# Performance work log

Hardware: AMD Instinct MI355X
Metric: run time of the kernel (lower is better)

## Reference

```python
import jax, jax.numpy as jnp
import numpy as np
from jax import lax

B, N, NPOINT, NSAMPLE = 16, 8192, 1024, 32
RADIUS = 0.2
EPS = 1e-5


def setup_inputs() -> dict:
    key = jax.random.key(0)
    ks = jax.random.split(key, 6)
    return {
        "xyz": jax.random.uniform(ks[0], (B, N, 3), dtype=jnp.float32),
        "points": jax.random.normal(ks[1], (B, N, 64), dtype=jnp.float32),
        "w1": jax.random.normal(ks[2], (64, 67), dtype=jnp.float32) * 0.1,
        "b1": jnp.zeros((64,), jnp.float32),
        "g1": jnp.ones((64,), jnp.float32),
        "be1": jnp.zeros((64,), jnp.float32),
        "w2": jax.random.normal(ks[3], (64, 64), dtype=jnp.float32) * 0.1,
        "b2": jnp.zeros((64,), jnp.float32),
        "g2": jnp.ones((64,), jnp.float32),
        "be2": jnp.zeros((64,), jnp.float32),
        "w3": jax.random.normal(ks[4], (128, 64), dtype=jnp.float32) * 0.1,
        "b3": jnp.zeros((128,), jnp.float32),
        "g3": jnp.ones((128,), jnp.float32),
        "be3": jnp.zeros((128,), jnp.float32),
    }


def farthest_point_sample(xyz, npoint):
    # Sequential FPS; deterministic start at index 0 (torch uses a random start).
    b, n, _ = xyz.shape
    batch_ix = jnp.arange(b)

    def step(carry, _):
        distance, farthest = carry
        centroid = xyz[batch_ix, farthest]              # [B,3]
        dist = jnp.sum((xyz - centroid[:, None, :]) ** 2, -1)  # [B,N]
        distance = jnp.minimum(distance, dist)
        return (distance, jnp.argmax(distance, -1).astype(jnp.int32)), farthest

    init = (jnp.full((b, n), 1e10, jnp.float32), jnp.zeros((b,), jnp.int32))
    _, idxs = lax.scan(step, init, None, length=npoint)
    return idxs.T                                        # [B,npoint]


def gather_points(points, idx):
    # points [B,N,C], idx [B,...] -> [B,...,C]
    return jax.vmap(lambda p, i: p[i])(points, idx)


def query_ball_point(radius, nsample, xyz, new_xyz):
    b, n, _ = xyz.shape
    sqrd = jnp.sum((new_xyz[:, :, None, :] - xyz[:, None, :, :]) ** 2, -1)  # [B,S,N]
    gidx = jnp.where(sqrd > radius ** 2, n, jnp.arange(n, dtype=jnp.int32)[None, None, :])
    gidx = jnp.sort(gidx, axis=-1)[:, :, :nsample]       # [B,S,K]
    first = gidx[:, :, :1]
    return jnp.where(gidx == n, first, gidx)


def conv_bn_relu(x, w, b, g, be):
    # x [B,C,S,K]; 1x1 conv == channel matmul, then train-mode BN over (B,S,K).
    y = jnp.einsum("bcsk,oc->bosk", x, w) + b[None, :, None, None]
    mean = jnp.mean(y, axis=(0, 2, 3), keepdims=True)
    var = jnp.mean((y - mean) ** 2, axis=(0, 2, 3), keepdims=True)
    yhat = (y - mean) * lax.rsqrt(var + EPS)
    return jax.nn.relu(yhat * g[None, :, None, None] + be[None, :, None, None])


def reference(xyz, points, w1, b1, g1, be1, w2, b2, g2, be2, w3, b3, g3, be3):
    fps_idx = farthest_point_sample(xyz, NPOINT)          # [B,S]
    new_xyz = gather_points(xyz, fps_idx)                 # [B,S,3]
    idx = query_ball_point(RADIUS, NSAMPLE, xyz, new_xyz) # [B,S,K]
    grouped_xyz = gather_points(xyz, idx)                 # [B,S,K,3]
    grouped_xyz_norm = grouped_xyz - new_xyz[:, :, None, :]
    grouped_points = gather_points(points, idx)           # [B,S,K,64]
    new_points = jnp.concatenate([grouped_xyz_norm, grouped_points], axis=-1)
    x = jnp.transpose(new_points, (0, 3, 1, 2))           # [B,67,S,K]
    x = conv_bn_relu(x, w1, b1, g1, be1)
    x = conv_bn_relu(x, w2, b2, g2, be2)
    x = conv_bn_relu(x, w3, b3, g3, be3)
    new_points_out = jnp.max(x, axis=-1)                  # [B,128,S]
    return new_xyz, new_points_out
```

## Files before the change

kernel.cpp:

```cpp
#include <hip/hip_runtime.h>
#include <hip/hip_bf16.h>

typedef unsigned short u16;
typedef unsigned long long u64;
typedef __attribute__((ext_vector_type(8))) short short8;
typedef __attribute__((ext_vector_type(4))) float f32x4;

#define NN 8192
#define SSAMP 1024
#define KK 32
#define NT_F 524288.0f
#define EPSV 1e-5f

__device__ __forceinline__ u64 umax64(u64 a, u64 b) { return a > b ? a : b; }

template <int C>
__device__ __forceinline__ void dppstep(unsigned& hi, unsigned& lo) {
  unsigned h2 = (unsigned)__builtin_amdgcn_update_dpp(0, (int)hi, C, 0xF, 0xF, true);
  unsigned l2 = (unsigned)__builtin_amdgcn_update_dpp(0, (int)lo, C, 0xF, 0xF, true);
  u64 a = ((u64)hi << 32) | lo;
  u64 b = ((u64)h2 << 32) | l2;
  bool g = b > a;
  hi = g ? h2 : hi;
  lo = g ? l2 : lo;
}

__device__ __forceinline__ u64 wave_max_key(u64 key) {
  unsigned hi = (unsigned)(key >> 32), lo = (unsigned)key;
  dppstep<0x111>(hi, lo);
  dppstep<0x112>(hi, lo);
  dppstep<0x114>(hi, lo);
  dppstep<0x118>(hi, lo);
  dppstep<0x142>(hi, lo);
  dppstep<0x143>(hi, lo);
  return ((u64)hi << 32) | lo;
}

__device__ __forceinline__ int morton3(int ix, int iy, int iz) {
  int m = (((ix >> 0) & 1) << 2) | (((iy >> 0) & 1) << 1) | (((iz >> 0) & 1) << 0);
  m |= (((ix >> 1) & 1) << 5) | (((iy >> 1) & 1) << 4) | (((iz >> 1) & 1) << 3);
  m |= (((ix >> 2) & 1) << 8) | (((iy >> 2) & 1) << 7) | (((iz >> 2) & 1) << 6);
  return m;
}

__global__ __launch_bounds__(1024, 1) void fps_bucket_kernel(const float* __restrict__ xyz,
                                                             float* __restrict__ newxyz) {
  extern __shared__ float dynls[];
  float* sx = dynls;
  float* sy = dynls + NN;
  float* sz = dynls + 2 * NN;
  int* sI = (int*)(dynls + 3 * NN);
  __shared__ int cnt[512], off[512];
  __shared__ u64 cand[2][16];
  __shared__ int pos0_sh;

  const int b = blockIdx.x, t = threadIdx.x;
  const float* base = xyz + (size_t)b * NN * 3;

  float px[8], py[8], pz[8];
  int pc[8];
  if (t < 512) cnt[t] = 0;
  __syncthreads();
#pragma unroll
  for (int j = 0; j < 8; j++) {
    int p = j * 1024 + t;
    px[j] = base[p * 3 + 0];
    py[j] = base[p * 3 + 1];
    pz[j] = base[p * 3 + 2];
    int ix = min(7, (int)(px[j] * 8.0f));
    int iy = min(7, (int)(py[j] * 8.0f));
    int iz = min(7, (int)(pz[j] * 8.0f));
    pc[j] = morton3(ix, iy, iz);
    atomicAdd(&cnt[pc[j]], 1);
  }
  __syncthreads();
  int myc = (t < 512) ? cnt[t] : 0;
  for (int st = 1; st < 512; st <<= 1) {
    int v = 0;
    if (t < 512) { v = cnt[t]; if (t >= st) v += cnt[t - st]; }
    __syncthreads();
    if (t < 512) cnt[t] = v;
    __syncthreads();
  }
  if (t < 512) off[t] = cnt[t] - myc;
  __syncthreads();
#pragma unroll
  for (int j = 0; j < 8; j++) {
    int pos = atomicAdd(&off[pc[j]], 1);
    sx[pos] = px[j]; sy[pos] = py[j]; sz[pos] = pz[j];
    int orig = j * 1024 + t;
    sI[pos] = orig;
    if (orig == 0) pos0_sh = pos;
  }
  __syncthreads();
  float X[8], Y[8], Z[8], D[8];
  unsigned L26[8];
  float lox = 1e30f, loy = 1e30f, loz = 1e30f;
  float hix = -1e30f, hiy = -1e30f, hiz = -1e30f;
#pragma unroll
  for (int j = 0; j < 8; j++) {
    int p = t * 8 + j;
    float x = sx[p], y = sy[p], z = sz[p];
    X[j] = x; Y[j] = y; Z[j] = z; D[j] = 1e10f;
    int orig = sI[p];
    L26[j] = ((unsigned)(8191 - orig) << 13) | (unsigned)p;
    lox = fminf(lox, x); hix = fmaxf(hix, x);
    loy = fminf(loy, y); hiy = fmaxf(hiy, y);
    loz = fminf(loz, z); hiz = fmaxf(hiz, z);
  }
  int cur = pos0_sh;
  const int w = t >> 6;
  u64 ckey = 0;
  float cbd = 1e30f;
  u64 wkeyS = 0;

  for (int it = 0; it < SSAMP; it++) {
    float cx = sx[cur], cy = sy[cur], cz = sz[cur];
    if (t == 0) {
      float* o = newxyz + ((size_t)b * SSAMP + it) * 3;
      o[0] = cx; o[1] = cy; o[2] = cz;
    }
    float ddx = fmaxf(fmaxf(lox - cx, cx - hix), 0.f);
    float ddy = fmaxf(fmaxf(loy - cy, cy - hiy), 0.f);
    float ddz = fmaxf(fmaxf(loz - cz, cz - hiz), 0.f);
    float lb2 = fmaf(ddx, ddx, fmaf(ddy, ddy, ddz * ddz));
    bool upd = lb2 <= fmaf(cbd, 1.0001f, 1e-12f);
    u64 act = __ballot(upd);
    if (act) {
      if (upd) {
        u64 k = 0;
        float bd = -1.0f;
#pragma unroll
        for (int j = 0; j < 8; j++) {
          float dx = __fsub_rn(X[j], cx);
          float dy = __fsub_rn(Y[j], cy);
          float dz = __fsub_rn(Z[j], cz);
          float d = __fadd_rn(__fadd_rn(__fmul_rn(dx, dx), __fmul_rn(dy, dy)), __fmul_rn(dz, dz));
          float dm = fminf(D[j], d);
          D[j] = dm;
          bd = fmaxf(bd, dm);
          u64 kj = ((u64)__float_as_uint(dm) << 26) | (u64)L26[j];
          k = umax64(k, kj);
        }
        ckey = k;
        cbd = bd;
      }
      u64 r = wave_max_key(ckey);
      unsigned rl = __builtin_amdgcn_readlane((int)(unsigned)r, 63);
      unsigned rh = __builtin_amdgcn_readlane((int)(unsigned)(r >> 32), 63);
      wkeyS = ((u64)rh << 32) | rl;
    }
    const int s = it & 1;
    if ((t & 63) == 0) cand[s][w] = wkeyS;
    __syncthreads();
    u64 v = cand[s][t & 15];
    unsigned vhi = (unsigned)(v >> 32), vlo = (unsigned)v;
    dppstep<0x111>(vhi, vlo);
    dppstep<0x112>(vhi, vlo);
    dppstep<0x114>(vhi, vlo);
    dppstep<0x118>(vhi, vlo);
    unsigned bl = __builtin_amdgcn_readlane((int)vlo, 15);
    cur = (int)(bl & 0x1FFFu);
  }
}

__global__ __launch_bounds__(512, 1) void fps_fallback_kernel(const float* __restrict__ xyz,
                                                              float* __restrict__ newxyz) {
  const int b = blockIdx.x, t = threadIdx.x;
  const float* base = xyz + (size_t)b * NN * 3;
  __shared__ u64 cand[2][8];
  float X[16], Y[16], Z[16], D[16];
#pragma unroll
  for (int j = 0; j < 16; j++) {
    int p = j * 512 + t;
    X[j] = base[p * 3 + 0];
    Y[j] = base[p * 3 + 1];
    Z[j] = base[p * 3 + 2];
    D[j] = 1e10f;
  }
  __syncthreads();
  int cur = 0;
  const int w = t >> 6;
  for (int it = 0; it < SSAMP; it++) {
    float cx = base[cur * 3 + 0];
    float cy = base[cur * 3 + 1];
    float cz = base[cur * 3 + 2];
    if (t == 0) {
      float* o = newxyz + ((size_t)b * SSAMP + it) * 3;
      o[0] = cx; o[1] = cy; o[2] = cz;
    }
    float bestd = -1.0f;
    int bj = 0;
#pragma unroll
    for (int j = 0; j < 16; j++) {
      float dx = __fsub_rn(X[j], cx);
      float dy = __fsub_rn(Y[j], cy);
      float dz = __fsub_rn(Z[j], cz);
      float d = __fadd_rn(__fadd_rn(__fmul_rn(dx, dx), __fmul_rn(dy, dy)), __fmul_rn(dz, dz));
      float dm = fminf(D[j], d);
      D[j] = dm;
      bool g = dm > bestd;
      bestd = g ? dm : bestd;
      bj = g ? j : bj;
    }
    u64 key = ((u64)__float_as_uint(bestd) << 32) |
              (u64)(unsigned)~(unsigned)(bj * 512 + t);
    key = wave_max_key(key);
    const int s = it & 1;
    if ((t & 63) == 63) cand[s][w] = key;
    __syncthreads();
    u64 c0 = cand[s][0], c1 = cand[s][1], c2 = cand[s][2], c3 = cand[s][3];
    u64 c4 = cand[s][4], c5 = cand[s][5], c6 = cand[s][6], c7 = cand[s][7];
    u64 a0 = umax64(c0, c1), a1 = umax64(c2, c3), a2 = umax64(c4, c5), a3 = umax64(c6, c7);
    u64 best = umax64(umax64(a0, a1), umax64(a2, a3));
    cur = (int)(~(unsigned)(best & 0xFFFFFFFFull));
  }
}

__global__ __launch_bounds__(256) void ballq_kernel(const float* __restrict__ xyz,
                                                    const float* __restrict__ newxyz,
                                                    int* __restrict__ ballidx) {
  const int wid = blockIdx.x * 4 + (threadIdx.x >> 6);
  const int lane = threadIdx.x & 63;
  const int b = wid >> 10;
  const float* base = xyz + (size_t)b * NN * 3;
  const float cx = newxyz[wid * 3 + 0];
  const float cy = newxyz[wid * 3 + 1];
  const float cz = newxyz[wid * 3 + 2];
  int* op = ballidx + (size_t)wid * KK;
  int cnt = 0, first = -1;
  for (int p0 = 0; p0 < NN; p0 += 64) {
    const int p = p0 + lane;
    float dx = __fsub_rn(cx, base[p * 3 + 0]);
    float dy = __fsub_rn(cy, base[p * 3 + 1]);
    float dz = __fsub_rn(cz, base[p * 3 + 2]);
    float d = __fadd_rn(__fadd_rn(__fmul_rn(dx, dx), __fmul_rn(dy, dy)), __fmul_rn(dz, dz));
    bool hit = d <= 0.04f;
    u64 m = __ballot(hit);
    if (m) {
      if (first < 0) first = p0 + __ffsll((long long)m) - 1;
      int rank = __popcll(m & ((1ull << lane) - 1ull));
      int slot = cnt + rank;
      if (hit && slot < KK) op[slot] = p;
      cnt += __popcll(m);
      if (cnt >= KK) break;
    }
  }
  if (cnt < KK && lane >= cnt && lane < KK) op[lane] = first;
}

__device__ __forceinline__ void stage_W(const float* __restrict__ w, float* Ws, int K, int O, int t) {
  for (int i2 = t; i2 < K * O; i2 += 256) {
    int c = i2 / O, o = i2 % O;
    Ws[i2] = w[o * K + c];
  }
}

__global__ __launch_bounds__(256) void gemm1_kernel(const float* __restrict__ xyz,
                                                    const float* __restrict__ pts,
                                                    const float* __restrict__ w1,
                                                    const float* __restrict__ b1,
                                                    const float* __restrict__ newxyz,
                                                    const int* __restrict__ ballidx,
                                                    u16* __restrict__ Y1,
                                                    float* __restrict__ bkt) {
  __shared__ __align__(16) float As[67 * 64];
  __shared__ __align__(16) float Ws[67 * 64];
  __shared__ int sidx[64];
  __shared__ float snx[6];
  __shared__ float ssum[64], ssq[64];
  const int t = threadIdx.x, blk = blockIdx.x;
  const int pbase = blk * 64;
  const int g0 = pbase >> 5;
  const int b = g0 >> 10;
  if (t < 64) { sidx[t] = ballidx[pbase + t]; ssum[t] = 0.f; ssq[t] = 0.f; }
  if (t < 6) snx[t] = newxyz[(size_t)g0 * 3 + t];
  stage_W(w1, Ws, 67, 64, t);
  __syncthreads();
  {
    int r = t >> 2, q = t & 3;
    const float4* prow = (const float4*)(pts + ((size_t)b * NN + sidx[r]) * 64);
#pragma unroll
    for (int l = 0; l < 4; l++) {
      float4 v = prow[q * 4 + l];
      int c = 3 + q * 16 + l * 4;
      As[(c + 0) * 64 + r] = v.x;
      As[(c + 1) * 64 + r] = v.y;
      As[(c + 2) * 64 + r] = v.z;
      As[(c + 3) * 64 + r] = v.w;
    }
  }
  if (t < 64) {
    const float* xp = xyz + ((size_t)b * NN + sidx[t]) * 3;
    int g = t >> 5;
    As[0 * 64 + t] = xp[0] - snx[g * 3 + 0];
    As[1 * 64 + t] = xp[1] - snx[g * 3 + 1];
    As[2 * 64 + t] = xp[2] - snx[g * 3 + 2];
  }
  __syncthreads();
  const int i = t & 15, j = t >> 4;
  float acc[4][4];
#pragma unroll
  for (int a = 0; a < 4; a++)
#pragma unroll
    for (int c2 = 0; c2 < 4; c2++) acc[a][c2] = 0.f;
#pragma unroll 4
  for (int c = 0; c < 67; c++) {
    float4 a4 = *(const float4*)&As[c * 64 + i * 4];
    float4 w4 = *(const float4*)&Ws[c * 64 + j * 4];
    float av[4] = {a4.x, a4.y, a4.z, a4.w};
    float wv[4] = {w4.x, w4.y, w4.z, w4.w};
#pragma unroll
    for (int ii = 0; ii < 4; ii++)
#pragma unroll
      for (int jj = 0; jj < 4; jj++) acc[ii][jj] = fmaf(av[ii], wv[jj], acc[ii][jj]);
  }
  float bl[4];
#pragma unroll
  for (int jj = 0; jj < 4; jj++) bl[jj] = b1[j * 4 + jj];
#pragma unroll
  for (int ii = 0; ii < 4; ii++) {
    union { ushort4 u4; __hip_bfloat16 h[4]; } pk;
#pragma unroll
    for (int jj = 0; jj < 4; jj++) {
      float y = acc[ii][jj] + bl[jj];
      acc[ii][jj] = y;
      pk.h[jj] = __float2bfloat16(y);
    }
    *(ushort4*)&Y1[((size_t)(pbase + i * 4 + ii)) * 64 + j * 4] = pk.u4;
  }
#pragma unroll
  for (int jj = 0; jj < 4; jj++) {
    float s = 0.f, q2 = 0.f;
#pragma unroll
    for (int ii = 0; ii < 4; ii++) { float v = acc[ii][jj]; s += v; q2 += v * v; }
    atomicAdd(&ssum[j * 4 + jj], s);
    atomicAdd(&ssq[j * 4 + jj], q2);
  }
  __syncthreads();
  float* bb = bkt + (size_t)(blk & 63) * 512;
  if (t < 64) atomicAdd(&bb[t], ssum[t]);
  else if (t < 128) atomicAdd(&bb[64 + (t - 64)], ssq[t - 64]);
}

__global__ __launch_bounds__(256) void collapse_kernel(const float* __restrict__ bkt,
                                                       float* __restrict__ dst) {
  int e = blockIdx.x * 256 + threadIdx.x;
  float s = 0.f;
#pragma unroll 8
  for (int u = 0; u < 64; u++) s += bkt[u * 512 + e];
  dst[e] = s;
}

__device__ __forceinline__ short8 bn_pack8(const u16 h[8], const float* sS, const float* sT, int c0) {
  short8 r;
#pragma unroll
  for (int x = 0; x < 8; x++) {
    float f = __bfloat162float(*(const __hip_bfloat16*)&h[x]);
    f = fmaxf(fmaf(f, sS[c0 + x], sT[c0 + x]), 0.f);
    __hip_bfloat16 hb = __float2bfloat16(f);
    r[x] = *(const short*)&hb;
  }
  return r;
}

__device__ __forceinline__ short8 w_pack8(const float v[8]) {
  short8 r;
#pragma unroll
  for (int x = 0; x < 8; x++) {
    __hip_bfloat16 hb = __float2bfloat16(v[x]);
    r[x] = *(const short*)&hb;
  }
  return r;
}

__global__ __launch_bounds__(256) void gemm2_mfma_kernel(u16* __restrict__ Y,
                                                         const float* __restrict__ w2,
                                                         const float* __restrict__ b2,
                                                         const float* __restrict__ g1,
                                                         const float* __restrict__ be1,
                                                         const float* __restrict__ statsC,
                                                         float* __restrict__ bkt) {
  __shared__ __align__(16) short Af[8 * 64 * 8];
  __shared__ __align__(16) short Bf[8 * 64 * 8];
  __shared__ __align__(16) u16 Cs[64 * 72];
  __shared__ float sS[64], sT[64];
  __shared__ float sSum[64], sSq[64];
  const int t = threadIdx.x, blk = blockIdx.x;
  const int pbase = blk * 64;
  if (t < 64) {
    float mean = statsC[t] * (1.0f / NT_F);
    float var = statsC[64 + t] * (1.0f / NT_F) - mean * mean;
    float s = g1[t] * rsqrtf(var + EPSV);
    sS[t] = s;
    sT[t] = be1[t] - mean * s;
  }
  __syncthreads();
  {
    int r = t >> 2, q = t & 3;
    const uint4* yrow = (const uint4*)(Y + (size_t)(pbase + r) * 64);
    union { uint4 u; u16 h[8]; } v0, v1;
    v0.u = yrow[q * 2]; v1.u = yrow[q * 2 + 1];
    int c0 = q * 16;
    int kt = c0 >> 5, mt = r >> 4;
    int qp0 = (c0 >> 3) & 3, qp1 = ((c0 + 8) >> 3) & 3;
    *(short8*)&Af[(((mt << 1) | kt) * 64 + qp0 * 16 + (r & 15)) * 8] = bn_pack8(v0.h, sS, sT, c0);
    *(short8*)&Af[(((mt << 1) | kt) * 64 + qp1 * 16 + (r & 15)) * 8] = bn_pack8(v1.h, sS, sT, c0 + 8);
  }
  {
    int o = t >> 2, q = t & 3;
    const float* wrow = w2 + o * 64 + q * 16;
    float f0[8], f1[8];
#pragma unroll
    for (int x = 0; x < 8; x++) { f0[x] = wrow[x]; f1[x] = wrow[8 + x]; }
    int c0 = q * 16;
    int kt = c0 >> 5, nt = o >> 4;
    int qp0 = (c0 >> 3) & 3, qp1 = ((c0 + 8) >> 3) & 3;
    *(short8*)&Bf[(((nt << 1) | kt) * 64 + qp0 * 16 + (o & 15)) * 8] = w_pack8(f0);
    *(short8*)&Bf[(((nt << 1) | kt) * 64 + qp1 * 16 + (o & 15)) * 8] = w_pack8(f1);
  }
  __syncthreads();
  const int w = t >> 6, L = t & 63, q = L >> 4;
  const int nt = w;
  short8 b0 = *(const short8*)&Bf[((nt * 2 + 0) * 64 + L) * 8];
  short8 b1 = *(const short8*)&Bf[((nt * 2 + 1) * 64 + L) * 8];
  const int o = nt * 16 + (L & 15);
  const float bl = b2[o];
  f32x4 acc[4];
#pragma unroll
  for (int mt = 0; mt < 4; mt++) {
    acc[mt] = (f32x4){0.f, 0.f, 0.f, 0.f};
    short8 a0 = *(const short8*)&Af[((mt * 2 + 0) * 64 + L) * 8];
    short8 a1 = *(const short8*)&Af[((mt * 2 + 1) * 64 + L) * 8];
    acc[mt] = __builtin_amdgcn_mfma_f32_16x16x32_bf16(a0, b0, acc[mt], 0, 0, 0);
    acc[mt] = __builtin_amdgcn_mfma_f32_16x16x32_bf16(a1, b1, acc[mt], 0, 0, 0);
  }
  float s = 0.f, q2 = 0.f;
#pragma unroll
  for (int mt = 0; mt < 4; mt++) {
#pragma unroll
    for (int r = 0; r < 4; r++) {
      float y = acc[mt][r] + bl;
      s += y; q2 += y * y;
      __hip_bfloat16 hb = __float2bfloat16(y);
      Cs[(mt * 16 + q * 4 + r) * 72 + o] = *(const u16*)&hb;
    }
  }
  s += __shfl_xor(s, 16); s += __shfl_xor(s, 32);
  q2 += __shfl_xor(q2, 16); q2 += __shfl_xor(q2, 32);
  if (L < 16) { sSum[o] = s; sSq[o] = q2; }
  __syncthreads();
  {
    int r = t >> 2, qq = t & 3;
    uint4 c0 = *(const uint4*)&Cs[r * 72 + qq * 16];
    uint4 c1 = *(const uint4*)&Cs[r * 72 + qq * 16 + 8];
    uint4* yrow = (uint4*)(Y + (size_t)(pbase + r) * 64);
    yrow[qq * 2] = c0; yrow[qq * 2 + 1] = c1;
  }
  float* bb = bkt + (size_t)(blk & 63) * 512;
  if (t < 64) atomicAdd(&bb[128 + t], sSum[t]);
  else if (t < 128) atomicAdd(&bb[192 + (t - 64)], sSq[t - 64]);
}

__global__ __launch_bounds__(256) void conv3max_mfma_kernel(const u16* __restrict__ Y,
                                                            const float* __restrict__ w3,
                                                            const float* __restrict__ b3,
                                                            const float* __restrict__ g2,
                                                            const float* __restrict__ be2,
                                                            const float* __restrict__ statsC,
                                                            float* __restrict__ bkt,
                                                            float* __restrict__ gmax,
                                                            float* __restrict__ gmin) {
  __shared__ __align__(16) short Af[8 * 64 * 8];
  __shared__ __align__(16) short Bf[16 * 64 * 8];
  __shared__ float sS[64], sT[64];
  __shared__ float sSum[128], sSq[128];
  const int t = threadIdx.x, blk = blockIdx.x;
  const int pbase = blk * 64;
  if (t < 64) {
    float mean = statsC[128 + t] * (1.0f / NT_F);
    float var = statsC[192 + t] * (1.0f / NT_F) - mean * mean;
    float s = g2[t] * rsqrtf(var + EPSV);
    sS[t] = s;
    sT[t] = be2[t] - mean * s;
  }
  __syncthreads();
  {
    int r = t >> 2, q = t & 3;
    const uint4* yrow = (const uint4*)(Y + (size_t)(pbase + r) * 64);
    union { uint4 u; u16 h[8]; } v0, v1;
    v0.u = yrow[q * 2]; v1.u = yrow[q * 2 + 1];
    int c0 = q * 16;
    int kt = c0 >> 5, mt = r >> 4;
    int qp0 = (c0 >> 3) & 3, qp1 = ((c0 + 8) >> 3) & 3;
    *(short8*)&Af[(((mt << 1) | kt) * 64 + qp0 * 16 + (r & 15)) * 8] = bn_pack8(v0.h, sS, sT, c0);
    *(short8*)&Af[(((mt << 1) | kt) * 64 + qp1 * 16 + (r & 15)) * 8] = bn_pack8(v1.h, sS, sT, c0 + 8);
  }
  {
    int o = t >> 1, h = t & 1;
    const float* wrow = w3 + o * 64 + h * 32;
    int nt = o >> 4;
#pragma unroll
    for (int g = 0; g < 4; g++) {
      float f[8];
#pragma unroll
      for (int x = 0; x < 8; x++) f[x] = wrow[g * 8 + x];
      *(short8*)&Bf[(((nt << 1) | h) * 64 + g * 16 + (o & 15)) * 8] = w_pack8(f);
    }
  }
  __syncthreads();
  const int w = t >> 6, L = t & 63, q = L >> 4;
  f32x4 acc[2][4];
#pragma unroll
  for (int n = 0; n < 2; n++)
#pragma unroll
    for (int mt = 0; mt < 4; mt++) acc[n][mt] = (f32x4){0.f, 0.f, 0.f, 0.f};
  short8 bfr[2][2];
#pragma unroll
  for (int n = 0; n < 2; n++) {
    int nt = 2 * w + n;
    bfr[n][0] = *(const short8*)&Bf[((nt * 2 + 0) * 64 + L) * 8];
    bfr[n][1] = *(const short8*)&Bf[((nt * 2 + 1) * 64 + L) * 8];
  }
#pragma unroll
  for (int mt = 0; mt < 4; mt++) {
    short8 a0 = *(const short8*)&Af[((mt * 2 + 0) * 64 + L) * 8];
    short8 a1 = *(const short8*)&Af[((mt * 2 + 1) * 64 + L) * 8];
#pragma unroll
    for (int n = 0; n < 2; n++) {
      acc[n][mt] = __builtin_amdgcn_mfma_f32_16x16x32_bf16(a0, bfr[n][0], acc[n][mt], 0, 0, 0);
      acc[n][mt] = __builtin_amdgcn_mfma_f32_16x16x32_bf16(a1, bfr[n][1], acc[n][mt], 0, 0, 0);
    }
  }
#pragma unroll
  for (int n = 0; n < 2; n++) {
    int o = (2 * w + n) * 16 + (L & 15);
    float bl = b3[o];
    float s = 0.f, q2 = 0.f;
    float gmx[2] = {-1e30f, -1e30f}, gmn[2] = {1e30f, 1e30f};
#pragma unroll
    for (int mt = 0; mt < 4; mt++) {
      int g = mt >> 1;
#pragma unroll
      for (int r = 0; r < 4; r++) {
        float y = acc[n][mt][r] + bl;
        s += y; q2 += y * y;
        gmx[g] = fmaxf(gmx[g], y);
        gmn[g] = fminf(gmn[g], y);
      }
    }
    s += __shfl_xor(s, 16); s += __shfl_xor(s, 32);
    q2 += __shfl_xor(q2, 16); q2 += __shfl_xor(q2, 32);
#pragma unroll
    for (int g = 0; g < 2; g++) {
      gmx[g] = fmaxf(gmx[g], __shfl_xor(gmx[g], 16));
      gmx[g] = fmaxf(gmx[g], __shfl_xor(gmx[g], 32));
      gmn[g] = fminf(gmn[g], __shfl_xor(gmn[g], 16));
      gmn[g] = fminf(gmn[g], __shfl_xor(gmn[g], 32));
    }
    if (L < 16) {
      sSum[o] = s; sSq[o] = q2;
#pragma unroll
      for (int g = 0; g < 2; g++) {
        gmax[(size_t)(blk * 2 + g) * 128 + o] = gmx[g];
        gmin[(size_t)(blk * 2 + g) * 128 + o] = gmn[g];
      }
    }
  }
  __syncthreads();
  float* bb = bkt + (size_t)(blk & 63) * 512;
  if (t < 128) atomicAdd(&bb[256 + t], sSum[t]);
  else atomicAdd(&bb[384 + (t - 128)], sSq[t - 128]);
}

__global__ __launch_bounds__(256) void finalize_kernel(const float* __restrict__ gmax,
                                                       const float* __restrict__ gmin,
                                                       const float* __restrict__ statsC,
                                                       const float* __restrict__ g3,
                                                       const float* __restrict__ be3,
                                                       float* __restrict__ outf) {
  int gi = blockIdx.x * 256 + threadIdx.x;
  int s = gi & 1023;
  int o = (gi >> 10) & 127;
  int b = gi >> 17;
  float mean = statsC[256 + o] * (1.0f / NT_F);
  float var = statsC[384 + o] * (1.0f / NT_F) - mean * mean;
  float sc = g3[o] * rsqrtf(var + EPSV);
  float sh = be3[o] - mean * sc;
  size_t gidx = (size_t)(b * 1024 + s) * 128 + o;
  float v = sc > 0.f ? gmax[gidx] : gmin[gidx];
  outf[gi] = fmaxf(fmaf(v, sc, sh), 0.f);
}

extern "C" void kernel_launch(void* const* d_in, const int* in_sizes, int n_in,
                              void* d_out, int out_size, void* d_ws, size_t ws_size,
                              hipStream_t stream) {
  const float* xyz = (const float*)d_in[0];
  const float* pts = (const float*)d_in[1];
  const float* w1 = (const float*)d_in[2];
  const float* b1 = (const float*)d_in[3];
  const float* g1 = (const float*)d_in[4];
  const float* be1 = (const float*)d_in[5];
  const float* w2 = (const float*)d_in[6];
  const float* b2 = (const float*)d_in[7];
  const float* g2 = (const float*)d_in[8];
  const float* be2 = (const float*)d_in[9];
  const float* w3 = (const float*)d_in[10];
  const float* b3 = (const float*)d_in[11];
  const float* g3 = (const float*)d_in[12];
  const float* be3 = (const float*)d_in[13];

  float* out = (float*)d_out;
  float* newxyz = out;
  float* outfeat = out + 49152;

  char* ws = (char*)d_ws;
  int* ballidx = (int*)ws;
  float* bkt = (float*)(ws + (2 << 20));
  float* statsC = (float*)(ws + (2 << 20) + 131072);
  float* gmax = (float*)(ws + (4 << 20));
  float* gmin = (float*)(ws + (12 << 20));
  u16* Y = (u16*)(ws + (20 << 20));

  hipMemsetAsync(bkt, 0, 64 * 512 * sizeof(float), stream);

  bool use_bucket = false;
  {
    hipError_t e = hipFuncSetAttribute((const void*)fps_bucket_kernel,
                                       hipFuncAttributeMaxDynamicSharedMemorySize, 131072);
    if (e == hipSuccess) {
      int nb = 0;
      hipError_t e2 = hipOccupancyMaxActiveBlocksPerMultiprocessor(
          &nb, (const void*)fps_bucket_kernel, 1024, 131072);
      use_bucket = (e2 == hipSuccess && nb >= 1);
    }
  }
  if (use_bucket)
    fps_bucket_kernel<<<16, 1024, 131072, stream>>>(xyz, newxyz);
  else
    fps_fallback_kernel<<<16, 512, 0, stream>>>(xyz, newxyz);

  ballq_kernel<<<4096, 256, 0, stream>>>(xyz, newxyz, ballidx);
  gemm1_kernel<<<8192, 256, 0, stream>>>(xyz, pts, w1, b1, newxyz, ballidx, Y, bkt);
  collapse_kernel<<<2, 256, 0, stream>>>(bkt, statsC);
  gemm2_mfma_kernel<<<8192, 256, 0, stream>>>(Y, w2, b2, g1, be1, statsC, bkt);
  collapse_kernel<<<2, 256, 0, stream>>>(bkt, statsC);
  conv3max_mfma_kernel<<<8192, 256, 0, stream>>>(Y, w3, b3, g2, be2, statsC, bkt, gmax, gmin);
  collapse_kernel<<<2, 256, 0, stream>>>(bkt, statsC);
  finalize_kernel<<<8192, 256, 0, stream>>>(gmax, gmin, statsC, g3, be3, outfeat);
}
```

Measured before the change: 1.423 ms.

## Use shared atomicMax for FPS reduction, shuffle BN stats, tile finalize transpose

The FPS loop drops the per-wave candidate array and the DPP cross-wave reduction. Each wave instead does an atomicMax on a triple-buffered shared 64-bit key, which cuts one reduction stage from every one of the 1024 serial iterations. gemm1 swaps its shared-memory atomics plus extra barrier for a wave shuffle reduction followed by global atomics. finalize becomes a tiled transpose through padded shared memory, so gmax/gmin reads and output writes are coalesced, using 512 blocks instead of 8192. The FPS change relies on 64-bit shared atomicMax contention among 16 waves being cheaper than the old DPP reduction.

```diff
diff --git a/kernel.cpp b/kernel.cpp
--- a/kernel.cpp
+++ b/kernel.cpp
@@ -51,7 +51,7 @@
   float* sz = dynls + 2 * NN;
   int* sI = (int*)(dynls + 3 * NN);
   __shared__ int cnt[512], off[512];
-  __shared__ u64 cand[2][16];
+  __shared__ u64 candS[3];
   __shared__ int pos0_sh;
 
   const int b = blockIdx.x, t = threadIdx.x;
@@ -60,6 +60,7 @@
   float px[8], py[8], pz[8];
   int pc[8];
   if (t < 512) cnt[t] = 0;
+  if (t == 0) { candS[0] = 0; candS[1] = 0; candS[2] = 0; }
   __syncthreads();
 #pragma unroll
   for (int j = 0; j < 8; j++) {
@@ -109,12 +110,13 @@
     loz = fminf(loz, z); hiz = fmaxf(hiz, z);
   }
   int cur = pos0_sh;
-  const int w = t >> 6;
   u64 ckey = 0;
   float cbd = 1e30f;
   u64 wkeyS = 0;
+  int s = 0;
 
   for (int it = 0; it < SSAMP; it++) {
+    const int sn = (s == 2) ? 0 : s + 1;
     float cx = sx[cur], cy = sy[cur], cz = sz[cur];
     if (t == 0) {
       float* o = newxyz + ((size_t)b * SSAMP + it) * 3;
@@ -125,8 +127,7 @@
     float ddz = fmaxf(fmaxf(loz - cz, cz - hiz), 0.f);
     float lb2 = fmaf(ddx, ddx, fmaf(ddy, ddy, ddz * ddz));
     bool upd = lb2 <= fmaf(cbd, 1.0001f, 1e-12f);
-    u64 act = __ballot(upd);
-    if (act) {
+    if (__ballot(upd)) {
       if (upd) {
         u64 k = 0;
         float bd = -1.0f;
@@ -145,22 +146,13 @@
         ckey = k;
         cbd = bd;
       }
-      u64 r = wave_max_key(ckey);
-      unsigned rl = __builtin_amdgcn_readlane((int)(unsigned)r, 63);
-      unsigned rh = __builtin_amdgcn_readlane((int)(unsigned)(r >> 32), 63);
-      wkeyS = ((u64)rh << 32) | rl;
-    }
-    const int s = it & 1;
-    if ((t & 63) == 0) cand[s][w] = wkeyS;
+      wkeyS = wave_max_key(ckey);
+    }
+    if ((t & 63) == 63) atomicMax(&candS[s], wkeyS);
+    if (t == 0) candS[sn] = 0;
     __syncthreads();
-    u64 v = cand[s][t & 15];
-    unsigned vhi = (unsigned)(v >> 32), vlo = (unsigned)v;
-    dppstep<0x111>(vhi, vlo);
-    dppstep<0x112>(vhi, vlo);
-    dppstep<0x114>(vhi, vlo);
-    dppstep<0x118>(vhi, vlo);
-    unsigned bl = __builtin_amdgcn_readlane((int)vlo, 15);
-    cur = (int)(bl & 0x1FFFu);
+    cur = (int)(candS[s] & 0x1FFFull);
+    s = sn;
   }
 }
 
@@ -268,12 +260,11 @@
   __shared__ __align__(16) float Ws[67 * 64];
   __shared__ int sidx[64];
   __shared__ float snx[6];
-  __shared__ float ssum[64], ssq[64];
   const int t = threadIdx.x, blk = blockIdx.x;
   const int pbase = blk * 64;
   const int g0 = pbase >> 5;
   const int b = g0 >> 10;
-  if (t < 64) { sidx[t] = ballidx[pbase + t]; ssum[t] = 0.f; ssq[t] = 0.f; }
+  if (t < 64) sidx[t] = ballidx[pbase + t];
   if (t < 6) snx[t] = newxyz[(size_t)g0 * 3 + t];
   stage_W(w1, Ws, 67, 64, t);
   __syncthreads();
@@ -329,18 +320,30 @@
     }
     *(ushort4*)&Y1[((size_t)(pbase + i * 4 + ii)) * 64 + j * 4] = pk.u4;
   }
+  float sums[4], sqs[4];
 #pragma unroll
   for (int jj = 0; jj < 4; jj++) {
     float s = 0.f, q2 = 0.f;
 #pragma unroll
     for (int ii = 0; ii < 4; ii++) { float v = acc[ii][jj]; s += v; q2 += v * v; }
-    atomicAdd(&ssum[j * 4 + jj], s);
-    atomicAdd(&ssq[j * 4 + jj], q2);
-  }
-  __syncthreads();
-  float* bb = bkt + (size_t)(blk & 63) * 512;
-  if (t < 64) atomicAdd(&bb[t], ssum[t]);
-  else if (t < 128) atomicAdd(&bb[64 + (t - 64)], ssq[t - 64]);
+    sums[jj] = s; sqs[jj] = q2;
+  }
+#pragma unroll
+  for (int off = 1; off < 16; off <<= 1) {
+#pragma unroll
+    for (int jj = 0; jj < 4; jj++) {
+      sums[jj] += __shfl_xor(sums[jj], off);
+      sqs[jj] += __shfl_xor(sqs[jj], off);
+    }
+  }
+  if ((t & 15) == 0) {
+    float* bb = bkt + (size_t)(blk & 63) * 512;
+#pragma unroll
+    for (int jj = 0; jj < 4; jj++) {
+      atomicAdd(&bb[j * 4 + jj], sums[jj]);
+      atomicAdd(&bb[64 + j * 4 + jj], sqs[jj]);
+    }
+  }
 }
 
 __global__ __launch_bounds__(256) void collapse_kernel(const float* __restrict__ bkt,
@@ -579,17 +582,34 @@
                                                        const float* __restrict__ g3,
                                                        const float* __restrict__ be3,
                                                        float* __restrict__ outf) {
-  int gi = blockIdx.x * 256 + threadIdx.x;
-  int s = gi & 1023;
-  int o = (gi >> 10) & 127;
-  int b = gi >> 17;
-  float mean = statsC[256 + o] * (1.0f / NT_F);
-  float var = statsC[384 + o] * (1.0f / NT_F) - mean * mean;
-  float sc = g3[o] * rsqrtf(var + EPSV);
-  float sh = be3[o] - mean * sc;
-  size_t gidx = (size_t)(b * 1024 + s) * 128 + o;
-  float v = sc > 0.f ? gmax[gidx] : gmin[gidx];
-  outf[gi] = fmaxf(fmaf(v, sc, sh), 0.f);
+  __shared__ float smax[64 * 65], smin[64 * 65];
+  __shared__ float ssc[64], ssh[64];
+  const int t = threadIdx.x, blk = blockIdx.x;
+  const int b = blk >> 5, st = (blk >> 1) & 15, oh = blk & 1;
+  const int o0 = oh * 64, g0 = b * 1024 + st * 64;
+  if (t < 64) {
+    int o = o0 + t;
+    float mean = statsC[256 + o] * (1.0f / NT_F);
+    float var = statsC[384 + o] * (1.0f / NT_F) - mean * mean;
+    float sc = g3[o] * rsqrtf(var + EPSV);
+    ssc[t] = sc;
+    ssh[t] = be3[o] - mean * sc;
+  }
+  const int col = t & 63, rw = t >> 6;
+#pragma unroll
+  for (int k = 0; k < 16; k++) {
+    int r = k * 4 + rw;
+    smax[r * 65 + col] = gmax[(size_t)(g0 + r) * 128 + o0 + col];
+    smin[r * 65 + col] = gmin[(size_t)(g0 + r) * 128 + o0 + col];
+  }
+  __syncthreads();
+#pragma unroll
+  for (int k = 0; k < 16; k++) {
+    int o = k * 4 + rw;
+    float sc = ssc[o], sh = ssh[o];
+    float v = sc > 0.f ? smax[col * 65 + o] : smin[col * 65 + o];
+    outf[((size_t)(b * 128 + o0 + o)) * 1024 + st * 64 + col] = fmaxf(fmaf(v, sc, sh), 0.f);
+  }
 }
 
 extern "C" void kernel_launch(void* const* d_in, const int* in_sizes, int n_in,
@@ -647,5 +667,5 @@
   collapse_kernel<<<2, 256, 0, stream>>>(bkt, statsC);
   conv3max_mfma_kernel<<<8192, 256, 0, stream>>>(Y, w3, b3, g2, be2, statsC, bkt, gmax, gmin);
   collapse_kernel<<<2, 256, 0, stream>>>(bkt, statsC);
-  finalize_kernel<<<8192, 256, 0, stream>>>(gmax, gmin, statsC, g3, be3, outfeat);
-}
+  finalize_kernel<<<512, 256, 0, stream>>>(gmax, gmin, statsC, g3, be3, outfeat);
+}
```

Measured after the change: 1.324 ms. 7.0% less time.
